# Kernel optimization log

Measured on AMD Instinct MI355X. Metric: run time of the kernel, lower is better.

The kernel has to match this reference:

```python
import jax, jax.numpy as jnp
import numpy as np

B, S, E = 2, 2048, 2048
NQ, NKV, HD = 16, 4, 128
WINDOW = 512
ROPE_BASE = 10000.0


def _rope(x):
    # x: [B, H, S, HD], interleaved even/odd rotation
    half = HD // 2
    freqs = 1.0 / (ROPE_BASE ** (2.0 * jnp.arange(half, dtype=jnp.float32) / HD))
    pos = jnp.arange(x.shape[2], dtype=jnp.float32)
    ang = pos[:, None] * freqs[None, :]            # [S, HD/2]
    cos = jnp.cos(ang)[None, None].astype(x.dtype)  # [1,1,S,HD/2]
    sin = jnp.sin(ang)[None, None].astype(x.dtype)
    xe = x[..., 0::2]
    xo = x[..., 1::2]
    re = xe * cos - xo * sin
    ro = xe * sin + xo * cos
    return jnp.stack([re, ro], axis=-1).reshape(x.shape)


def setup_inputs() -> dict:
    key = jax.random.key(0)
    ks = jax.random.split(key, 9)
    s_in = 1.0 / np.sqrt(E)
    s_out = 1.0 / np.sqrt(NQ * HD)
    return {
        "x": jax.random.normal(ks[0], (B, S, E), jnp.float32),
        "Wq": jax.random.normal(ks[1], (E, NQ * HD), jnp.float32) * s_in,
        "bq": jax.random.normal(ks[2], (NQ * HD,), jnp.float32) * 0.01,
        "Wk": jax.random.normal(ks[3], (E, NKV * HD), jnp.float32) * s_in,
        "bk": jax.random.normal(ks[4], (NKV * HD,), jnp.float32) * 0.01,
        "Wv": jax.random.normal(ks[5], (E, NKV * HD), jnp.float32) * s_in,
        "bv": jax.random.normal(ks[6], (NKV * HD,), jnp.float32) * 0.01,
        "Wo": jax.random.normal(ks[7], (NQ * HD, E), jnp.float32) * s_out,
        "bo": jax.random.normal(ks[8], (E,), jnp.float32) * 0.01,
    }


def reference(x, Wq, bq, Wk, bk, Wv, bv, Wo, bo):
    b, s, _ = x.shape
    q = (x @ Wq + bq).reshape(b, s, NQ, HD).transpose(0, 2, 1, 3)   # [B,NQ,S,HD]
    k = (x @ Wk + bk).reshape(b, s, NKV, HD).transpose(0, 2, 1, 3)  # [B,NKV,S,HD]
    v = (x @ Wv + bv).reshape(b, s, NKV, HD).transpose(0, 2, 1, 3)
    q = _rope(q)
    k = _rope(k)
    rep = NQ // NKV
    k = jnp.repeat(k, rep, axis=1)  # [B,NQ,S,HD], matches torch repeat pattern
    v = jnp.repeat(v, rep, axis=1)
    scores = jnp.einsum("bhqd,bhkd->bhqk", q, k) / np.sqrt(HD)
    i = jnp.arange(s)[:, None]
    j = jnp.arange(s)[None, :]
    allowed = (j <= i) & ((i - j) <= WINDOW)  # sliding-window causal mask
    scores = jnp.where(allowed[None, None], scores, -jnp.inf)
    weights = jax.nn.softmax(scores, axis=-1)
    out = jnp.einsum("bhqk,bhkd->bhqd", weights, v)
    out = out.transpose(0, 2, 1, 3).reshape(b, s, NQ * HD)
    return out @ Wo + bo
```

## Files before the change

### kernel.cpp

```cpp
#include <hip/hip_runtime.h>
#include <hip/hip_bf16.h>
#include <math.h>

#define BB 2
#define SS 2048
#define EE 2048
#define NQ 16
#define NKV 4
#define HD 128
#define WINDOW 512

typedef __hip_bfloat16 bf16;
typedef short short8 __attribute__((ext_vector_type(8)));
typedef float f32x4 __attribute__((ext_vector_type(4)));

__device__ __forceinline__ float toF(bf16 v) { return __bfloat162float(v); }
__device__ __forceinline__ bf16 toB(float v) { return __float2bfloat16(v); }

__device__ __forceinline__ void gld_lds16(const void* g, void* l) {
    __builtin_amdgcn_global_load_lds(
        (const __attribute__((address_space(1))) void*)g,
        (__attribute__((address_space(3))) void*)l, 16, 0, 0);
}

__global__ __launch_bounds__(256) void convert_bf16(const float* __restrict__ in,
                                                    bf16* __restrict__ out, int n) {
    int i = (blockIdx.x * 256 + threadIdx.x) * 4;
    if (i >= n) return;
    const float4 v = *(const float4*)(in + i);
    bf16 o[4] = {toB(v.x), toB(v.y), toB(v.z), toB(v.w)};
    *(uint2*)(out + i) = *(const uint2*)o;
}

__global__ __launch_bounds__(256) void convert_transpose(const float* __restrict__ in,
                                                         bf16* __restrict__ out,
                                                         int K, int N) {
    __shared__ float tile[32][33];
    const int t = threadIdx.x;
    const int tx = t & 31, ty = t >> 5;
    const int n0 = blockIdx.x * 32, k0 = blockIdx.y * 32;
#pragma unroll
    for (int r = 0; r < 4; r++)
        tile[ty + r * 8][tx] = in[(size_t)(k0 + ty + r * 8) * N + n0 + tx];
    __syncthreads();
#pragma unroll
    for (int r = 0; r < 4; r++)
        out[(size_t)(n0 + ty + r * 8) * K + k0 + tx] = toB(tile[tx][ty + r * 8]);
}

__global__ __launch_bounds__(256) void convert_transpose_qkv(
    const float* __restrict__ Wq, const float* __restrict__ Wk,
    const float* __restrict__ Wv, bf16* __restrict__ out) {
    __shared__ float tile[32][33];
    const int t = threadIdx.x;
    const int tx = t & 31, ty = t >> 5;
    const int n0 = blockIdx.x * 32, k0 = blockIdx.y * 32;
    const float* src; int N, nl0;
    if (n0 < 2048)      { src = Wq; N = 2048; nl0 = n0; }
    else if (n0 < 2560) { src = Wk; N = 512;  nl0 = n0 - 2048; }
    else                { src = Wv; N = 512;  nl0 = n0 - 2560; }
#pragma unroll
    for (int r = 0; r < 4; r++)
        tile[ty + r * 8][tx] = src[(size_t)(k0 + ty + r * 8) * N + nl0 + tx];
    __syncthreads();
#pragma unroll
    for (int r = 0; r < 4; r++)
        out[(size_t)(n0 + ty + r * 8) * 2048 + k0 + tx] = toB(tile[tx][ty + r * 8]);
}

template <int MODE>
__global__ __launch_bounds__(256) void mfma_gemm(
    const bf16* __restrict__ A, const bf16* __restrict__ BT,
    const float* __restrict__ b0, const float* __restrict__ b1,
    const float* __restrict__ b2,
    float* __restrict__ Yf,
    bf16* __restrict__ Yq, bf16* __restrict__ Yk, bf16* __restrict__ Yv,
    int M, int N, int K) {
    __shared__ bf16 As[128 * 32];
    __shared__ bf16 Bs[128 * 32];

    const int t = threadIdx.x;
    const int lane = t & 63;
    const int w = t >> 6;
    const int wm = w >> 1, wn = w & 1;
    const int m0 = blockIdx.y * 128, n0 = blockIdx.x * 128;

    const int srow = lane >> 2;
    const int sg   = lane & 3;
    const int scol = (sg ^ ((srow >> 1) & 3)) * 8;

    f32x4 acc[4][4];
#pragma unroll
    for (int i = 0; i < 4; i++)
#pragma unroll
        for (int j = 0; j < 4; j++) acc[i][j] = (f32x4)0.f;

    const int lr = lane & 15;
    const int lq = lane >> 4;
    const int slotr = (lq ^ ((lr >> 1) & 3)) * 8;

    for (int k0 = 0; k0 < K; k0 += 32) {
#pragma unroll
        for (int s = 0; s < 2; s++) {
            const int c = w * 2 + s;
            gld_lds16(A + (size_t)(m0 + c * 16 + srow) * K + k0 + scol, As + c * 512);
            gld_lds16(BT + (size_t)(n0 + c * 16 + srow) * K + k0 + scol, Bs + c * 512);
        }
        __syncthreads();
        short8 af[4], bfv[4];
#pragma unroll
        for (int i = 0; i < 4; i++)
            af[i] = *(const short8*)(As + (wm * 64 + i * 16 + lr) * 32 + slotr);
#pragma unroll
        for (int j = 0; j < 4; j++)
            bfv[j] = *(const short8*)(Bs + (wn * 64 + j * 16 + lr) * 32 + slotr);
#pragma unroll
        for (int i = 0; i < 4; i++)
#pragma unroll
            for (int j = 0; j < 4; j++)
                acc[i][j] = __builtin_amdgcn_mfma_f32_16x16x32_bf16(af[i], bfv[j],
                                                                    acc[i][j], 0, 0, 0);
        __syncthreads();
    }

    if (MODE == 0) {
#pragma unroll
        for (int j = 0; j < 4; j++) {
            const int col = n0 + wn * 64 + j * 16 + lr;
            const float bj = b0[col];
#pragma unroll
            for (int i = 0; i < 4; i++) {
                const int row = m0 + wm * 64 + i * 16 + lq * 4;
#pragma unroll
                for (int r = 0; r < 4; r++)
                    Yf[(size_t)(row + r) * N + col] = acc[i][j][r] + bj;
            }
        }
    } else {
        bf16* outp; const float* bias; int ldc, c0; bool dorope;
        if (n0 < 2048)      { outp = Yq; bias = b0; ldc = 2048; c0 = n0;        dorope = true; }
        else if (n0 < 2560) { outp = Yk; bias = b1; ldc = 512;  c0 = n0 - 2048; dorope = true; }
        else                { outp = Yv; bias = b2; ldc = 512;  c0 = n0 - 2560; dorope = false; }
#pragma unroll
        for (int j = 0; j < 4; j++) {
            const int col = c0 + wn * 64 + j * 16 + lr;
            const float bj = bias[col];
            if (dorope) {
                const int d2 = (col & 127) >> 1;
                const bool odd = col & 1;
                const float freq = __expf(-0.14384103622589045f * (float)d2);
#pragma unroll
                for (int i = 0; i < 4; i++) {
                    const int row = m0 + wm * 64 + i * 16 + lq * 4;
#pragma unroll
                    for (int r = 0; r < 4; r++) {
                        const float v = acc[i][j][r] + bj;
                        const float p = __shfl_xor(v, 1, 64);
                        const float ang = (float)((row + r) & (SS - 1)) * freq;
                        float sn, cs;
                        __sincosf(ang, &sn, &cs);
                        const float o = odd ? (p * sn + v * cs) : (v * cs - p * sn);
                        outp[(size_t)(row + r) * ldc + col] = toB(o);
                    }
                }
            } else {
#pragma unroll
                for (int i = 0; i < 4; i++) {
                    const int row = m0 + wm * 64 + i * 16 + lq * 4;
#pragma unroll
                    for (int r = 0; r < 4; r++)
                        outp[(size_t)(row + r) * ldc + col] = toB(acc[i][j][r] + bj);
                }
            }
        }
    }
}

__global__ __launch_bounds__(256) void attn_mfma(const bf16* __restrict__ Q,
                                                 const bf16* __restrict__ K,
                                                 const bf16* __restrict__ V,
                                                 bf16* __restrict__ Oout) {
    __shared__ bf16 Ks[64 * 128];
    __shared__ bf16 Vt[128 * 72];
    __shared__ bf16 Ps[4 * 16 * 72];

    const int t = threadIdx.x;
    const int lane = t & 63;
    const int w = t >> 6;
    const int q0 = blockIdx.x * 64;
    const int h = blockIdx.y;
    const int b = blockIdx.z;
    const int hkv = h >> 2;
    const int lr = lane & 15;
    const int lq = lane >> 4;
    const float scale = 0.08838834764831845f;

    short8 aq[4];
    {
        const int q = q0 + w * 16 + lr;
        const bf16* qp = Q + (((size_t)b * SS + q) * NQ + h) * HD + lq * 8;
#pragma unroll
        for (int ks = 0; ks < 4; ks++) aq[ks] = *(const short8*)(qp + ks * 32);
    }

    f32x4 Oa[8];
#pragma unroll
    for (int nb = 0; nb < 8; nb++) Oa[nb] = (f32x4)0.f;
    float mprev[4] = {-3.0e38f, -3.0e38f, -3.0e38f, -3.0e38f};
    float lsum[4] = {0.f, 0.f, 0.f, 0.f};

    bf16* Pw = Ps + w * 16 * 72;
    const int jstart = (q0 >= WINDOW) ? (q0 - WINDOW) : 0;

    for (int c0 = jstart; c0 <= q0; c0 += 64) {
        __syncthreads();
#pragma unroll
        for (int s = 0; s < 4; s++) {
            const bf16* gk = K +
                (((size_t)b * SS + c0 + w * 16 + s * 4 + (lane >> 4)) * NKV + hkv) * HD +
                (lane & 15) * 8;
            gld_lds16(gk, Ks + (w * 16 + s * 4) * 128);
        }
        {
            const int key = t & 63;
            const int dg = (t >> 6) * 8;
            const bf16* gv = V + (((size_t)b * SS + c0 + key) * NKV + hkv) * HD + dg;
#pragma unroll
            for (int it = 0; it < 4; it++) {
                short8 vv = *(const short8*)(gv + it * 32);
#pragma unroll
                for (int j = 0; j < 8; j++)
                    Vt[(dg + it * 32 + j) * 72 + key] = ((const bf16*)&vv)[j];
            }
        }
        __syncthreads();

        f32x4 sa[4];
#pragma unroll
        for (int nb = 0; nb < 4; nb++) sa[nb] = (f32x4)0.f;
#pragma unroll
        for (int ks = 0; ks < 4; ks++) {
#pragma unroll
            for (int nb = 0; nb < 4; nb++) {
                short8 bk = *(const short8*)(Ks + (nb * 16 + lr) * 128 + ks * 32 + lq * 8);
                sa[nb] = __builtin_amdgcn_mfma_f32_16x16x32_bf16(aq[ks], bk, sa[nb], 0, 0, 0);
            }
        }

        const int rowb = q0 + w * 16 + lq * 4;
        float pr[4][4], alpha[4];
#pragma unroll
        for (int r = 0; r < 4; r++) {
            const int row = rowb + r;
            float sv[4];
            float mx = -3.0e38f;
#pragma unroll
            for (int nb = 0; nb < 4; nb++) {
                const int col = c0 + nb * 16 + lr;
                const bool valid = (col <= row) && (row - col <= WINDOW);
                const float s = valid ? sa[nb][r] * scale : -3.0e38f;
                sv[nb] = s;
                mx = fmaxf(mx, s);
            }
#pragma unroll
            for (int off = 1; off < 16; off <<= 1) mx = fmaxf(mx, __shfl_xor(mx, off, 64));
            const float mn = fmaxf(fmaxf(mprev[r], mx), -1.0e30f);
            alpha[r] = __expf(mprev[r] - mn);
            mprev[r] = mn;
            float rs = 0.f;
#pragma unroll
            for (int nb = 0; nb < 4; nb++) {
                const float p = __expf(sv[nb] - mn);
                pr[r][nb] = p;
                rs += p;
            }
#pragma unroll
            for (int off = 1; off < 16; off <<= 1) rs += __shfl_xor(rs, off, 64);
            lsum[r] = lsum[r] * alpha[r] + rs;
        }

#pragma unroll
        for (int r = 0; r < 4; r++)
#pragma unroll
            for (int nb = 0; nb < 4; nb++)
                Pw[(lq * 4 + r) * 72 + nb * 16 + lr] = toB(pr[r][nb]);

#pragma unroll
        for (int nb = 0; nb < 8; nb++)
#pragma unroll
            for (int r = 0; r < 4; r++) Oa[nb][r] *= alpha[r];
#pragma unroll
        for (int ks = 0; ks < 2; ks++) {
            short8 pa = *(const short8*)(Pw + lr * 72 + ks * 32 + lq * 8);
#pragma unroll
            for (int nb = 0; nb < 8; nb++) {
                short8 bv = *(const short8*)(Vt + (nb * 16 + lr) * 72 + ks * 32 + lq * 8);
                Oa[nb] = __builtin_amdgcn_mfma_f32_16x16x32_bf16(pa, bv, Oa[nb], 0, 0, 0);
            }
        }
    }

    float linv[4];
#pragma unroll
    for (int r = 0; r < 4; r++) linv[r] = 1.f / lsum[r];
    const int rowb = q0 + w * 16 + lq * 4;
#pragma unroll
    for (int nb = 0; nb < 8; nb++)
#pragma unroll
        for (int r = 0; r < 4; r++)
            Oout[(((size_t)b * SS + rowb + r) * NQ + h) * HD + nb * 16 + lr] =
                toB(Oa[nb][r] * linv[r]);
}

extern "C" void kernel_launch(void* const* d_in, const int* in_sizes, int n_in,
                              void* d_out, int out_size, void* d_ws, size_t ws_size,
                              hipStream_t stream) {
    const float* x  = (const float*)d_in[0];
    const float* Wq = (const float*)d_in[1];
    const float* bq = (const float*)d_in[2];
    const float* Wk = (const float*)d_in[3];
    const float* bk = (const float*)d_in[4];
    const float* Wv = (const float*)d_in[5];
    const float* bv = (const float*)d_in[6];
    const float* Wo = (const float*)d_in[7];
    const float* bo = (const float*)d_in[8];
    float* out = (float*)d_out;

    const int M   = BB * SS;
    const int DQ  = NQ * HD;
    const int DKV = NKV * HD;
    const int NPK = DQ + 2 * DKV;

    bf16* xb     = (bf16*)d_ws;
    bf16* WqkvT  = xb + (size_t)M * EE;
    bf16* WoT    = WqkvT + (size_t)NPK * EE;
    bf16* Qb     = WoT + (size_t)EE * DQ;
    bf16* Kb     = Qb + (size_t)M * DQ;
    bf16* Vb     = Kb + (size_t)M * DKV;

    convert_bf16<<<(M * EE / 4 + 255) / 256, 256, 0, stream>>>(x, xb, M * EE);
    convert_transpose_qkv<<<dim3(NPK / 32, EE / 32), 256, 0, stream>>>(Wq, Wk, Wv, WqkvT);
    convert_transpose<<<dim3(DQ / 32, DQ / 32), 256, 0, stream>>>(Wo, WoT, DQ, EE);

    mfma_gemm<1><<<dim3(NPK / 128, M / 128), 256, 0, stream>>>(
        xb, WqkvT, bq, bk, bv, nullptr, Qb, Kb, Vb, M, NPK, EE);

    attn_mfma<<<dim3(SS / 64, NQ, BB), 256, 0, stream>>>(Qb, Kb, Vb, Qb);

    mfma_gemm<0><<<dim3(EE / 128, M / 128), 256, 0, stream>>>(
        Qb, WoT, bo, nullptr, nullptr, out, nullptr, nullptr, nullptr, M, EE, DQ);
}
```

Before: 329.4 us.

## Store V transposed from QKV GEMM and async-load swizzled K/V tiles

The QKV GEMM epilogue now writes V directly in a [b, kv_head, d, seq] transposed layout, and it folds the softmax scale into Q. The attention kernel then loads both K and V tiles with direct global-to-LDS async loads using an XOR swizzle, replacing the per-element LDS transpose scatter of V. Mask evaluation is skipped for tiles that lie fully inside the causal window. The changes aim to cut LDS bank conflicts, scalar LDS stores and mask ALU work in attention. The price is strided 8-byte stores in the GEMM epilogue and some rounding difference from pre-scaling Q before bf16 conversion.

```diff
diff --git a/kernel.cpp b/kernel.cpp
--- a/kernel.cpp
+++ b/kernel.cpp
@@ -136,41 +136,49 @@
                     Yf[(size_t)(row + r) * N + col] = acc[i][j][r] + bj;
             }
         }
-    } else {
-        bf16* outp; const float* bias; int ldc, c0; bool dorope;
-        if (n0 < 2048)      { outp = Yq; bias = b0; ldc = 2048; c0 = n0;        dorope = true; }
-        else if (n0 < 2560) { outp = Yk; bias = b1; ldc = 512;  c0 = n0 - 2048; dorope = true; }
-        else                { outp = Yv; bias = b2; ldc = 512;  c0 = n0 - 2560; dorope = false; }
+    } else if (n0 < 2560) {
+        bf16* outp; const float* bias; int ldc, c0; float oscale;
+        if (n0 < 2048) { outp = Yq; bias = b0; ldc = 2048; c0 = n0;
+                         oscale = 0.08838834764831845f; }
+        else           { outp = Yk; bias = b1; ldc = 512;  c0 = n0 - 2048;
+                         oscale = 1.0f; }
 #pragma unroll
         for (int j = 0; j < 4; j++) {
             const int col = c0 + wn * 64 + j * 16 + lr;
             const float bj = bias[col];
-            if (dorope) {
-                const int d2 = (col & 127) >> 1;
-                const bool odd = col & 1;
-                const float freq = __expf(-0.14384103622589045f * (float)d2);
-#pragma unroll
-                for (int i = 0; i < 4; i++) {
-                    const int row = m0 + wm * 64 + i * 16 + lq * 4;
-#pragma unroll
-                    for (int r = 0; r < 4; r++) {
-                        const float v = acc[i][j][r] + bj;
-                        const float p = __shfl_xor(v, 1, 64);
-                        const float ang = (float)((row + r) & (SS - 1)) * freq;
-                        float sn, cs;
-                        __sincosf(ang, &sn, &cs);
-                        const float o = odd ? (p * sn + v * cs) : (v * cs - p * sn);
-                        outp[(size_t)(row + r) * ldc + col] = toB(o);
-                    }
+            const int d2 = (col & 127) >> 1;
+            const bool odd = col & 1;
+            const float freq = __expf(-0.14384103622589045f * (float)d2);
+#pragma unroll
+            for (int i = 0; i < 4; i++) {
+                const int row = m0 + wm * 64 + i * 16 + lq * 4;
+#pragma unroll
+                for (int r = 0; r < 4; r++) {
+                    const float v = acc[i][j][r] + bj;
+                    const float p = __shfl_xor(v, 1, 64);
+                    const float ang = (float)((row + r) & (SS - 1)) * freq;
+                    float sn, cs;
+                    __sincosf(ang, &sn, &cs);
+                    const float o = odd ? (p * sn + v * cs) : (v * cs - p * sn);
+                    outp[(size_t)(row + r) * ldc + col] = toB(o * oscale);
                 }
-            } else {
-#pragma unroll
-                for (int i = 0; i < 4; i++) {
-                    const int row = m0 + wm * 64 + i * 16 + lq * 4;
-#pragma unroll
-                    for (int r = 0; r < 4; r++)
-                        outp[(size_t)(row + r) * ldc + col] = toB(acc[i][j][r] + bj);
-                }
+            }
+        }
+    } else {
+#pragma unroll
+        for (int j = 0; j < 4; j++) {
+            const int colv = (n0 - 2560) + wn * 64 + j * 16 + lr;
+            const float bj = b2[colv];
+            const int hv = colv >> 7, d = colv & 127;
+#pragma unroll
+            for (int i = 0; i < 4; i++) {
+                const int row = m0 + wm * 64 + i * 16 + lq * 4;
+                const int bb2 = row >> 11, sloc = row & (SS - 1);
+                bf16 pk[4];
+#pragma unroll
+                for (int r = 0; r < 4; r++) pk[r] = toB(acc[i][j][r] + bj);
+                *(uint2*)(Yv + (((size_t)bb2 * NKV + hv) * HD + d) * SS + sloc) =
+                    *(const uint2*)pk;
             }
         }
     }
@@ -178,10 +186,10 @@
 
 __global__ __launch_bounds__(256) void attn_mfma(const bf16* __restrict__ Q,
                                                  const bf16* __restrict__ K,
-                                                 const bf16* __restrict__ V,
+                                                 const bf16* __restrict__ Vt_g,
                                                  bf16* __restrict__ Oout) {
     __shared__ bf16 Ks[64 * 128];
-    __shared__ bf16 Vt[128 * 72];
+    __shared__ bf16 Vt[128 * 64];
     __shared__ bf16 Ps[4 * 16 * 72];
 
     const int t = threadIdx.x;
@@ -193,7 +201,6 @@
     const int hkv = h >> 2;
     const int lr = lane & 15;
     const int lq = lane >> 4;
-    const float scale = 0.08838834764831845f;
 
     short8 aq[4];
     {
@@ -211,27 +218,25 @@
 
     bf16* Pw = Ps + w * 16 * 72;
     const int jstart = (q0 >= WINDOW) ? (q0 - WINDOW) : 0;
+    const bf16* Vrow = Vt_g + ((size_t)b * NKV + hkv) * HD * SS;
 
     for (int c0 = jstart; c0 <= q0; c0 += 64) {
         __syncthreads();
 #pragma unroll
         for (int s = 0; s < 4; s++) {
-            const bf16* gk = K +
-                (((size_t)b * SS + c0 + w * 16 + s * 4 + (lane >> 4)) * NKV + hkv) * HD +
-                (lane & 15) * 8;
-            gld_lds16(gk, Ks + (w * 16 + s * 4) * 128);
-        }
-        {
-            const int key = t & 63;
-            const int dg = (t >> 6) * 8;
-            const bf16* gv = V + (((size_t)b * SS + c0 + key) * NKV + hkv) * HD + dg;
-#pragma unroll
-            for (int it = 0; it < 4; it++) {
-                short8 vv = *(const short8*)(gv + it * 32);
-#pragma unroll
-                for (int j = 0; j < 8; j++)
-                    Vt[(dg + it * 32 + j) * 72 + key] = ((const bf16*)&vv)[j];
-            }
+            const int kr = w * 16 + s * 4 + (lane >> 4);
+            const int sl = lane & 15;
+            const int g = (sl & 8) | ((sl & 7) ^ (kr & 7));
+            gld_lds16(K + (((size_t)b * SS + c0 + kr) * NKV + hkv) * HD + g * 8,
+                      Ks + (w * 16 + s * 4) * 128);
+        }
+#pragma unroll
+        for (int s = 0; s < 4; s++) {
+            const int dr = w * 32 + s * 8 + (lane >> 3);
+            const int sl = lane & 7;
+            const int g = sl ^ (dr & 7);
+            gld_lds16(Vrow + (size_t)dr * SS + c0 + g * 8,
+                      Vt + (w * 32 + s * 8) * 64);
         }
         __syncthreads();
 
@@ -242,25 +247,37 @@
         for (int ks = 0; ks < 4; ks++) {
 #pragma unroll
             for (int nb = 0; nb < 4; nb++) {
-                short8 bk = *(const short8*)(Ks + (nb * 16 + lr) * 128 + ks * 32 + lq * 8);
+                const int row = nb * 16 + lr;
+                const int g = ks * 4 + lq;
+                const int slot = (g & 8) | ((g & 7) ^ (row & 7));
+                short8 bk = *(const short8*)(Ks + row * 128 + slot * 8);
                 sa[nb] = __builtin_amdgcn_mfma_f32_16x16x32_bf16(aq[ks], bk, sa[nb], 0, 0, 0);
             }
         }
 
         const int rowb = q0 + w * 16 + lq * 4;
+        const bool needmask = !((c0 + 63 <= q0 + w * 16) &&
+                                (q0 + w * 16 + 15 - c0 <= WINDOW));
         float pr[4][4], alpha[4];
 #pragma unroll
         for (int r = 0; r < 4; r++) {
             const int row = rowb + r;
             float sv[4];
             float mx = -3.0e38f;
-#pragma unroll
-            for (int nb = 0; nb < 4; nb++) {
-                const int col = c0 + nb * 16 + lr;
-                const bool valid = (col <= row) && (row - col <= WINDOW);
-                const float s = valid ? sa[nb][r] * scale : -3.0e38f;
-                sv[nb] = s;
-                mx = fmaxf(mx, s);
+            if (needmask) {
+#pragma unroll
+                for (int nb = 0; nb < 4; nb++) {
+                    const int col = c0 + nb * 16 + lr;
+                    const bool valid = (col <= row) && (row - col <= WINDOW);
+                    sv[nb] = valid ? sa[nb][r] : -3.0e38f;
+                    mx = fmaxf(mx, sv[nb]);
+                }
+            } else {
+#pragma unroll
+                for (int nb = 0; nb < 4; nb++) {
+                    sv[nb] = sa[nb][r];
+                    mx = fmaxf(mx, sv[nb]);
+                }
             }
 #pragma unroll
             for (int off = 1; off < 16; off <<= 1) mx = fmaxf(mx, __shfl_xor(mx, off, 64));
@@ -294,7 +311,10 @@
             short8 pa = *(const short8*)(Pw + lr * 72 + ks * 32 + lq * 8);
 #pragma unroll
             for (int nb = 0; nb < 8; nb++) {
-                short8 bv = *(const short8*)(Vt + (nb * 16 + lr) * 72 + ks * 32 + lq * 8);
+                const int d = nb * 16 + lr;
+                const int g = ks * 4 + lq;
+                const int slot = g ^ (d & 7);
+                short8 bv = *(const short8*)(Vt + d * 64 + slot * 8);
                 Oa[nb] = __builtin_amdgcn_mfma_f32_16x16x32_bf16(pa, bv, Oa[nb], 0, 0, 0);
             }
         }
@@ -336,16 +356,16 @@
     bf16* WoT    = WqkvT + (size_t)NPK * EE;
     bf16* Qb     = WoT + (size_t)EE * DQ;
     bf16* Kb     = Qb + (size_t)M * DQ;
-    bf16* Vb     = Kb + (size_t)M * DKV;
+    bf16* Vtg    = Kb + (size_t)M * DKV;
 
     convert_bf16<<<(M * EE / 4 + 255) / 256, 256, 0, stream>>>(x, xb, M * EE);
     convert_transpose_qkv<<<dim3(NPK / 32, EE / 32), 256, 0, stream>>>(Wq, Wk, Wv, WqkvT);
     convert_transpose<<<dim3(DQ / 32, DQ / 32), 256, 0, stream>>>(Wo, WoT, DQ, EE);
 
     mfma_gemm<1><<<dim3(NPK / 128, M / 128), 256, 0, stream>>>(
-        xb, WqkvT, bq, bk, bv, nullptr, Qb, Kb, Vb, M, NPK, EE);
-
-    attn_mfma<<<dim3(SS / 64, NQ, BB), 256, 0, stream>>>(Qb, Kb, Vb, Qb);
+        xb, WqkvT, bq, bk, bv, nullptr, Qb, Kb, Vtg, M, NPK, EE);
+
+    attn_mfma<<<dim3(SS / 64, NQ, BB), 256, 0, stream>>>(Qb, Kb, Vtg, Qb);
 
     mfma_gemm<0><<<dim3(EE / 128, M / 128), 256, 0, stream>>>(
         Qb, WoT, bo, nullptr, nullptr, out, nullptr, nullptr, nullptr, M, EE, DQ);
```

New measurement: 332.7 us. No clear change (+1.0%).
